# Kernel tuning notes

Measured on AMD Instinct MI355X. Metric: run time of the kernel, lower is better.

Reference implementation:

```python
import jax, jax.numpy as jnp
import numpy as np

HEADS = 30
HEAD_DIM = 64
DIM = HEADS * HEAD_DIM  # 1920
TXT = 226
VID = 2048
EPS = 1e-5


def setup_inputs() -> dict:
    key = jax.random.key(0)
    ks = jax.random.split(key, 12)
    s = 1.0 / np.sqrt(DIM)
    return {
        "hidden_states": jax.random.normal(ks[0], (1, VID, DIM), jnp.float32),
        "encoder_hidden_states": jax.random.normal(ks[1], (1, TXT, DIM), jnp.float32),
        "rope_cos": jax.random.uniform(ks[2], (VID, HEAD_DIM), jnp.float32, -1.0, 1.0),
        "rope_sin": jax.random.uniform(ks[3], (VID, HEAD_DIM), jnp.float32, -1.0, 1.0),
        "Wq": jax.random.normal(ks[4], (DIM, DIM), jnp.float32) * s,
        "bq": jnp.zeros((DIM,), jnp.float32),
        "Wk": jax.random.normal(ks[5], (DIM, DIM), jnp.float32) * s,
        "bk": jnp.zeros((DIM,), jnp.float32),
        "Wv": jax.random.normal(ks[6], (DIM, DIM), jnp.float32) * s,
        "bv": jnp.zeros((DIM,), jnp.float32),
        "ln_q_w": jnp.ones((HEAD_DIM,), jnp.float32),
        "ln_q_b": jnp.zeros((HEAD_DIM,), jnp.float32),
        "ln_k_w": jnp.ones((HEAD_DIM,), jnp.float32),
        "ln_k_b": jnp.zeros((HEAD_DIM,), jnp.float32),
        "Wo": jax.random.normal(ks[7], (DIM, DIM), jnp.float32) * s,
        "bo": jnp.zeros((DIM,), jnp.float32),
    }


def _layernorm(x, w, b):
    mu = jnp.mean(x, axis=-1, keepdims=True)
    var = jnp.var(x, axis=-1, keepdims=True)
    return (x - mu) * jax.lax.rsqrt(var + EPS) * w + b


def _apply_rope(x, cos, sin):
    # x: [B,H,S_vid,D]; cos/sin: [S_vid,D]. Interleaved-pair rotation (diffusers use_real, unbind_dim=-1).
    xr = x[..., 0::2]
    xi = x[..., 1::2]
    rot = jnp.stack([-xi, xr], axis=-1).reshape(x.shape)
    return x * cos + rot * sin


def reference(hidden_states, encoder_hidden_states, rope_cos, rope_sin,
              Wq, bq, Wk, bk, Wv, bv, ln_q_w, ln_q_b, ln_k_w, ln_k_b, Wo, bo):
    T = encoder_hidden_states.shape[1]
    h = jnp.concatenate([encoder_hidden_states, hidden_states], axis=1)  # [B,S,D]
    B, S, _ = h.shape

    def proj(W, bias):
        y = h @ W.T + bias
        return y.reshape(B, S, HEADS, HEAD_DIM).transpose(0, 2, 1, 3)  # [B,H,S,d]

    q = proj(Wq, bq)
    k = proj(Wk, bk)
    v = proj(Wv, bv)

    q = _layernorm(q, ln_q_w, ln_q_b)
    k = _layernorm(k, ln_k_w, ln_k_b)

    # rotary embedding applied only to the image/video tokens
    q = jnp.concatenate([q[:, :, :T], _apply_rope(q[:, :, T:], rope_cos, rope_sin)], axis=2)
    k = jnp.concatenate([k[:, :, :T], _apply_rope(k[:, :, T:], rope_cos, rope_sin)], axis=2)

    scale = 1.0 / np.sqrt(HEAD_DIM)
    scores = jnp.einsum("bhqd,bhkd->bhqk", q, k) * scale
    attn = jax.nn.softmax(scores, axis=-1)
    out = jnp.einsum("bhqk,bhkd->bhqd", attn, v)

    out = out.transpose(0, 2, 1, 3).reshape(B, S, DIM)
    out = out @ Wo.T + bo
    return out[:, T:], out[:, :T]
```

## Files before the change

### kernel.cpp

```cpp
#include <hip/hip_runtime.h>
#include <hip/hip_bf16.h>

typedef __hip_bfloat16 bf16;
using f32x4 = __attribute__((ext_vector_type(4))) float;
using f32x16 = __attribute__((ext_vector_type(16))) float;
using s16x8 = __attribute__((ext_vector_type(8))) short;

#define S_TOT 2274
#define S_PAD 2304
#define TTXT 226
#define DIMN 1920
#define NH 30
#define HD 64
#define NQKV 5760
#define QSCALE 0.1803368801f
#define NSPLIT 3
#define SMAX 20.0f

#define GLOAD_LDS16(g, l)                                                              \
  __builtin_amdgcn_global_load_lds((const __attribute__((address_space(1))) void*)(g), \
                                   (__attribute__((address_space(3))) void*)(l), 16, 0, 0)

__global__ void k_prep_all(const float* __restrict__ hid, const float* __restrict__ enc,
                           const float* __restrict__ Wq, const float* __restrict__ Wk,
                           const float* __restrict__ Wv, const float* __restrict__ Wo,
                           bf16* __restrict__ h_bf, bf16* __restrict__ wqkv,
                           bf16* __restrict__ wo_bf) {
  const long T1 = (long)S_PAD * DIMN;
  const long PER = (long)DIMN * DIMN;
  long i4 = ((long)blockIdx.x * blockDim.x + threadIdx.x) * 4;
  if (i4 >= T1 + 4 * PER) return;
  float4 v = make_float4(0.f, 0.f, 0.f, 0.f);
  bf16* dst;
  long di;
  if (i4 < T1) {
    int s = (int)(i4 / DIMN);
    if (s < TTXT)
      v = *reinterpret_cast<const float4*>(enc + i4);
    else if (s < S_TOT)
      v = *reinterpret_cast<const float4*>(hid + i4 - (long)TTXT * DIMN);
    dst = h_bf;
    di = i4;
  } else if (i4 < T1 + 3 * PER) {
    const long j = i4 - T1;
    const float* src = (j < PER) ? (Wq + j) : (j < 2 * PER) ? (Wk + j - PER) : (Wv + j - 2 * PER);
    v = *reinterpret_cast<const float4*>(src);
    dst = wqkv;
    di = j;
  } else {
    const long j = i4 - T1 - 3 * PER;
    v = *reinterpret_cast<const float4*>(Wo + j);
    dst = wo_bf;
    di = j;
  }
  union {
    bf16 b[4];
    short4 s4;
  } o;
  o.b[0] = __float2bfloat16(v.x);
  o.b[1] = __float2bfloat16(v.y);
  o.b[2] = __float2bfloat16(v.z);
  o.b[3] = __float2bfloat16(v.w);
  *reinterpret_cast<short4*>(dst + di) = o.s4;
}

#define NKT32 60
#define QBUF 24576
__global__ __launch_bounds__(512, 4) void k_gemm_qkv9(
    const bf16* __restrict__ A, const bf16* __restrict__ B, const float* __restrict__ bq,
    const float* __restrict__ bk, const float* __restrict__ bv, const float* __restrict__ lqw,
    const float* __restrict__ lqb, const float* __restrict__ lkw, const float* __restrict__ lkb,
    const float* __restrict__ cosT, const float* __restrict__ sinT, bf16* __restrict__ qb,
    bf16* __restrict__ kbf, bf16* __restrict__ vt) {
  __shared__ __align__(16) char smem[3 * QBUF];
  const int tid = threadIdx.x;
  const int w = tid >> 6, lane = tid & 63;
  const int clo = lane & 15, lhi = lane >> 4;
  const int wr = w >> 1, wc = w & 1;
  const int m0 = blockIdx.y * 256, n0 = blockIdx.x * 128;

  const int u1 = 512 + tid;
  const long ga0 = (long)(m0 + (tid >> 2)) * DIMN + (((tid & 3) ^ ((tid >> 2) & 3)) * 8);
  const long ga1 = (long)(m0 + (u1 >> 2)) * DIMN + (((u1 & 3) ^ ((u1 >> 2) & 3)) * 8);
  const long gb0 = (long)(n0 + (tid >> 2)) * DIMN + (((tid & 3) ^ ((tid >> 2) & 3)) * 8);
  const int wbase = w * 1024;

  auto stage = [&](int b, int kt) {
    char* Ab = &smem[b * QBUF];
    char* Bb = Ab + 16384;
    const int ko = kt * 32;
    GLOAD_LDS16(A + ga0 + ko, Ab + wbase);
    GLOAD_LDS16(A + ga1 + ko, Ab + 8192 + wbase);
    GLOAD_LDS16(B + gb0 + ko, Bb + wbase);
  };

  auto rdf = [&](const char* base, int row) {
    return *reinterpret_cast<const s16x8*>(base + row * 64 + ((lhi ^ (row & 3)) * 16));
  };

  f32x4 acc[4][4] = {};

  stage(0, 0);
  stage(1, 1);
  for (int t = 0; t < NKT32; ++t) {
    if (t < NKT32 - 1)
      asm volatile("s_waitcnt vmcnt(3)" ::: "memory");
    else
      asm volatile("s_waitcnt vmcnt(0)" ::: "memory");
    __builtin_amdgcn_s_barrier();
    if (t + 2 < NKT32) stage((t + 2) % 3, t + 2);
    const char* Ab = &smem[(t % 3) * QBUF];
    const char* Bb = Ab + 16384;
    s16x8 af[4], bfr[4];
#pragma unroll
    for (int m = 0; m < 4; ++m) af[m] = rdf(Ab, wr * 64 + m * 16 + clo);
#pragma unroll
    for (int n = 0; n < 4; ++n) bfr[n] = rdf(Bb, wc * 64 + n * 16 + clo);
    __builtin_amdgcn_s_setprio(1);
#pragma unroll
    for (int m = 0; m < 4; ++m)
#pragma unroll
      for (int n = 0; n < 4; ++n)
        acc[m][n] = __builtin_amdgcn_mfma_f32_16x16x32_bf16(af[m], bfr[n], acc[m][n], 0, 0, 0);
    __builtin_amdgcn_s_setprio(0);
  }
  __syncthreads();

  const int gcol0 = n0 + wc * 64;
  const int sect = gcol0 / DIMN;
  const int hcol = gcol0 - sect * DIMN;
  const int head = hcol >> 6;
  const int row0 = m0 + wr * 64;

  if (sect < 2) {
    const float* bias = sect ? bk : bq;
    const float* lw = sect ? lkw : lqw;
    const float* lb = sect ? lkb : lqb;
    bf16* dst = sect ? kbf : qb;
    const float oscale = sect ? 1.f : QSCALE;
    float bb[4], lww[4], lbb[4];
#pragma unroll
    for (int n = 0; n < 4; ++n) {
      const int d = (n << 4) + clo;
      bb[n] = bias[hcol + d];
      lww[n] = lw[d];
      lbb[n] = lb[d];
    }
#pragma unroll
    for (int m = 0; m < 4; ++m) {
#pragma unroll
      for (int r = 0; r < 4; ++r) {
        const int row = row0 + m * 16 + lhi * 4 + r;
        float x[4];
#pragma unroll
        for (int n = 0; n < 4; ++n) x[n] = acc[m][n][r] + bb[n];
        float s_ = (x[0] + x[1]) + (x[2] + x[3]);
        float q_ = x[0] * x[0];
        q_ = fmaf(x[1], x[1], q_);
        q_ = fmaf(x[2], x[2], q_);
        q_ = fmaf(x[3], x[3], q_);
#pragma unroll
        for (int off = 1; off <= 8; off <<= 1) {
          s_ += __shfl_xor(s_, off);
          q_ += __shfl_xor(q_, off);
        }
        const float mu = s_ * (1.f / 64.f);
        const float var = q_ * (1.f / 64.f) - mu * mu;
        const float rst = rsqrtf(var + 1e-5f);
        float xn[4];
#pragma unroll
        for (int n = 0; n < 4; ++n) xn[n] = (x[n] - mu) * rst * lww[n] + lbb[n];
        const bool dorope = (row >= TTXT) && (row < S_TOT);
        if (dorope) {
          const float* cr = cosT + (long)(row - TTXT) * HD;
          const float* sr2 = sinT + (long)(row - TTXT) * HD;
#pragma unroll
          for (int n = 0; n < 4; ++n) {
            const int d = (n << 4) + clo;
            const float p = __shfl_xor(xn[n], 1);
            xn[n] = xn[n] * cr[d] + ((clo & 1) ? p : -p) * sr2[d];
          }
        }
#pragma unroll
        for (int n = 0; n < 4; ++n)
          dst[((long)head * S_PAD + row) * HD + (n << 4) + clo] =
              __float2bfloat16(xn[n] * oscale);
      }
    }
  } else {
    float bb[4];
#pragma unroll
    for (int n = 0; n < 4; ++n) bb[n] = bv[hcol + (n << 4) + clo];
    bf16* Lp = reinterpret_cast<bf16*>(smem + w * 9216);
#pragma unroll
    for (int m = 0; m < 4; ++m)
#pragma unroll
      for (int n = 0; n < 4; ++n)
#pragma unroll
        for (int r = 0; r < 4; ++r)
          Lp[((n << 4) + clo) * 72 + m * 16 + lhi * 4 + r] =
              __float2bfloat16(acc[m][n][r] + bb[n]);
    const int dsub = lane >> 3, sc = lane & 7;
#pragma unroll
    for (int it = 0; it < 8; ++it) {
      const int d = it * 8 + dsub;
      s16x8 v = *reinterpret_cast<const s16x8*>(&Lp[d * 72 + sc * 8]);
      *reinterpret_cast<s16x8*>(vt + ((long)head * HD + d) * S_PAD + row0 + sc * 8) = v;
    }
  }
}

__global__ __launch_bounds__(256, 4) void k_gemm_proj9(const bf16* __restrict__ A,
                                                       const bf16* __restrict__ B,
                                                       float* __restrict__ C,
                                                       const float* __restrict__ bias) {
  __shared__ __align__(16) char smem[3 * 12288];
  const int tid = threadIdx.x;
  const int w = tid >> 6, lane = tid & 63;
  const int clo = lane & 15, lhi = lane >> 4;
  const int wr = w >> 1, wc = w & 1;
  const int m0 = blockIdx.y * 128, n0 = blockIdx.x * 64;

  const int u1 = 256 + tid;
  const long ga0 = (long)(m0 + (tid >> 2)) * DIMN + (((tid & 3) ^ ((tid >> 2) & 3)) * 8);
  const long ga1 = (long)(m0 + (u1 >> 2)) * DIMN + (((u1 & 3) ^ ((u1 >> 2) & 3)) * 8);
  const long gb0 = (long)(n0 + (tid >> 2)) * DIMN + (((tid & 3) ^ ((tid >> 2) & 3)) * 8);
  const int wbase = w * 1024;

  auto stage = [&](int b, int kt) {
    char* Ab = &smem[b * 12288];
    char* Bb = Ab + 8192;
    const int ko = kt * 32;
    GLOAD_LDS16(A + ga0 + ko, Ab + wbase);
    GLOAD_LDS16(A + ga1 + ko, Ab + 4096 + wbase);
    GLOAD_LDS16(B + gb0 + ko, Bb + wbase);
  };

  auto rdf = [&](const char* base, int row) {
    return *reinterpret_cast<const s16x8*>(base + row * 64 + ((lhi ^ (row & 3)) * 16));
  };

  f32x4 acc[4][2] = {};

  stage(0, 0);
  stage(1, 1);
  for (int t = 0; t < NKT32; ++t) {
    if (t < NKT32 - 1)
      asm volatile("s_waitcnt vmcnt(3)" ::: "memory");
    else
      asm volatile("s_waitcnt vmcnt(0)" ::: "memory");
    __builtin_amdgcn_s_barrier();
    if (t + 2 < NKT32) stage((t + 2) % 3, t + 2);
    const char* Ab = &smem[(t % 3) * 12288];
    const char* Bb = Ab + 8192;
    s16x8 af[4], bfr[2];
#pragma unroll
    for (int m = 0; m < 4; ++m) af[m] = rdf(Ab, wr * 64 + m * 16 + clo);
#pragma unroll
    for (int n = 0; n < 2; ++n) bfr[n] = rdf(Bb, wc * 32 + n * 16 + clo);
    __builtin_amdgcn_s_setprio(1);
#pragma unroll
    for (int m = 0; m < 4; ++m)
#pragma unroll
      for (int n = 0; n < 2; ++n)
        acc[m][n] = __builtin_amdgcn_mfma_f32_16x16x32_bf16(af[m], bfr[n], acc[m][n], 0, 0, 0);
    __builtin_amdgcn_s_setprio(0);
  }
#pragma unroll
  for (int n = 0; n < 2; ++n) {
    const int col = n0 + wc * 32 + n * 16 + clo;
    const float bvv = bias[col];
#pragma unroll
    for (int m = 0; m < 4; ++m) {
#pragma unroll
      for (int r = 0; r < 4; ++r) {
        const int row = m0 + wr * 64 + m * 16 + lhi * 4 + r;
        if (row < S_TOT) {
          const int dst = (row >= TTXT) ? (row - TTXT) : (row + (S_TOT - TTXT));
          C[(long)dst * DIMN + col] = acc[m][n][r] + bvv;
        }
      }
    }
  }
}

__global__ __launch_bounds__(512, 4) void k_flash11(const bf16* __restrict__ qb,
                                                    const bf16* __restrict__ kbf,
                                                    const bf16* __restrict__ vt,
                                                    float* __restrict__ po,
                                                    float* __restrict__ pl) {
  __shared__ __align__(16) char smem[32768];
  const int h = blockIdx.x, qt = blockIdx.y, ks = blockIdx.z;
  const int tid = threadIdx.x, w = tid >> 6, lane = tid & 63;
  const int l31 = lane & 31, hf = lane >> 5;
  const bf16* Qh = qb + (long)h * S_PAD * HD;
  const bf16* Kh = kbf + (long)h * S_PAD * HD;
  const bf16* Vh = vt + (long)h * HD * S_PAD;
  const int q0w = qt * 256 + w * 32;
  const int T0 = ks * 12;

  s16x8 qf[4];
#pragma unroll
  for (int t = 0; t < 4; ++t)
    qf[t] = *reinterpret_cast<const s16x8*>(Qh + (long)(q0w + l31) * HD + t * 16 + hf * 8);

  f32x16 accO[2] = {};
  f32x16 lacc = {};

  const s16x8 ones8 = {0x3F80, 0x3F80, 0x3F80, 0x3F80, 0x3F80, 0x3F80, 0x3F80, 0x3F80};

  const int sr = tid >> 3, sc8 = tid & 7;
  const long kg0 = (long)sr * HD + ((sc8 ^ (sr & 7)) * 8);
  const long vg0 = (long)sr * S_PAD + ((sc8 ^ (sr & 7)) * 8);
  const int ldsb = w * 1024;

  auto stage = [&](int b, int kb0) {
    char* Kb = &smem[b * 16384];
    char* Vb = &smem[b * 16384 + 8192];
    GLOAD_LDS16(Kh + (long)kb0 * HD + kg0, Kb + ldsb);
    GLOAD_LDS16(Vh + kb0 + vg0, Vb + ldsb);
  };

  auto ldsrd = [&](const char* base, int row, int c) {
    return *reinterpret_cast<const s16x8*>(base + row * 128 + ((c ^ (row & 7)) * 16));
  };
  auto pk2 = [&](float a, float b) -> unsigned {
    __hip_bfloat162 t = __float22bfloat162_rn(make_float2(a, b));
    return *reinterpret_cast<unsigned*>(&t);
  };

  stage(0, T0 * 64);
  __syncthreads();
  int cur = 0;
  for (int kt = 0; kt < 12; ++kt) {
    const int kb0 = (T0 + kt) * 64;
    if (kt + 1 < 12) stage(cur ^ 1, kb0 + 64);
    const char* Kb = &smem[cur * 16384];
    const char* Vb = &smem[cur * 16384 + 8192];

    f32x16 s0 = {}, s1 = {};
#pragma unroll
    for (int t = 0; t < 4; ++t) {
      s16x8 k0 = ldsrd(Kb, l31, 2 * t + hf);
      s16x8 k1 = ldsrd(Kb, 32 + l31, 2 * t + hf);
      s0 = __builtin_amdgcn_mfma_f32_32x32x16_bf16(k0, qf[t], s0, 0, 0, 0);
      s1 = __builtin_amdgcn_mfma_f32_32x32x16_bf16(k1, qf[t], s1, 0, 0, 0);
    }
    if (kb0 + 64 > S_TOT) {
#pragma unroll
      for (int j = 0; j < 16; ++j) {
        const int key = kb0 + (j & 3) + 8 * (j >> 2) + 4 * hf;
        if (key >= S_TOT) s0[j] = -1e30f;
        if (key + 32 >= S_TOT) s1[j] = -1e30f;
      }
    }
#pragma unroll
    for (int j = 0; j < 16; ++j) {
      s0[j] = exp2f(s0[j] - SMAX);
      s1[j] = exp2f(s1[j] - SMAX);
    }
    unsigned gw0[8], gw1[8];
#pragma unroll
    for (int i = 0; i < 4; ++i) {
      gw0[2 * i] = pk2(s0[4 * i], s0[4 * i + 1]);
      gw0[2 * i + 1] = pk2(s0[4 * i + 2], s0[4 * i + 3]);
      gw1[2 * i] = pk2(s1[4 * i], s1[4 * i + 1]);
      gw1[2 * i + 1] = pk2(s1[4 * i + 2], s1[4 * i + 3]);
    }
    s16x8 pa[4];
#pragma unroll
    for (int b = 0; b < 2; ++b) {
      unsigned* gw = b ? gw1 : gw0;
#pragma unroll
      for (int t = 0; t < 2; ++t) {
        auto rA = __builtin_amdgcn_permlane32_swap(gw[4 * t + 0], gw[4 * t + 2], false, false);
        auto rB = __builtin_amdgcn_permlane32_swap(gw[4 * t + 1], gw[4 * t + 3], false, false);
        union {
          unsigned u[4];
          s16x8 v;
        } A;
        A.u[0] = rA[0];
        A.u[1] = rB[0];
        A.u[2] = rA[1];
        A.u[3] = rB[1];
        pa[b * 2 + t] = A.v;
      }
    }
#pragma unroll
    for (int t4 = 0; t4 < 4; ++t4) {
      s16x8 v0 = ldsrd(Vb, l31, 2 * t4 + hf);
      s16x8 v1 = ldsrd(Vb, 32 + l31, 2 * t4 + hf);
      accO[0] = __builtin_amdgcn_mfma_f32_32x32x16_bf16(pa[t4], v0, accO[0], 0, 0, 0);
      accO[1] = __builtin_amdgcn_mfma_f32_32x32x16_bf16(pa[t4], v1, accO[1], 0, 0, 0);
      lacc = __builtin_amdgcn_mfma_f32_32x32x16_bf16(pa[t4], ones8, lacc, 0, 0, 0);
    }
    __syncthreads();
    cur ^= 1;
  }
  const long rowbase = ((long)(ks * NH + h)) * S_PAD + q0w;
  if (l31 == 0) {
#pragma unroll
    for (int j = 0; j < 16; ++j) pl[rowbase + (j & 3) + 8 * (j >> 2) + 4 * hf] = lacc[j];
  }
#pragma unroll
  for (int j = 0; j < 16; ++j) {
    const int pat = (j & 3) + 8 * (j >> 2) + 4 * hf;
    float* dst = po + (rowbase + pat) * HD + l31;
    dst[0] = accO[0][j];
    dst[32] = accO[1][j];
  }
}

__global__ __launch_bounds__(256) void k_combine3(const float* __restrict__ po,
                                                  const float* __restrict__ pl,
                                                  bf16* __restrict__ ao) {
  const int idx = blockIdx.x * 256 + threadIdx.x;
  const int d4 = (idx & 15) * 4;
  const int row = (idx >> 4) % S_PAD;
  const int h = idx / (S_PAD * 16);
  if (row >= S_TOT) return;
  float4 o = make_float4(0.f, 0.f, 0.f, 0.f);
  float l = 0.f;
#pragma unroll
  for (int i = 0; i < NSPLIT; ++i) {
    const long r = ((long)(i * NH + h)) * S_PAD + row;
    const float4 p = *reinterpret_cast<const float4*>(po + r * HD + d4);
    o.x += p.x;
    o.y += p.y;
    o.z += p.z;
    o.w += p.w;
    l += pl[r];
  }
  const float inv = 1.f / l;
  union {
    bf16 b[4];
    short4 s4;
  } ob;
  ob.b[0] = __float2bfloat16(o.x * inv);
  ob.b[1] = __float2bfloat16(o.y * inv);
  ob.b[2] = __float2bfloat16(o.z * inv);
  ob.b[3] = __float2bfloat16(o.w * inv);
  *reinterpret_cast<short4*>(ao + (long)row * DIMN + h * HD + d4) = ob.s4;
}

extern "C" void kernel_launch(void* const* d_in, const int* in_sizes, int n_in, void* d_out,
                              int out_size, void* d_ws, size_t ws_size, hipStream_t stream) {
  const float* hid = (const float*)d_in[0];
  const float* enc = (const float*)d_in[1];
  const float* rc = (const float*)d_in[2];
  const float* rs = (const float*)d_in[3];
  const float* Wq = (const float*)d_in[4];
  const float* bq = (const float*)d_in[5];
  const float* Wk = (const float*)d_in[6];
  const float* bk = (const float*)d_in[7];
  const float* Wv = (const float*)d_in[8];
  const float* bv = (const float*)d_in[9];
  const float* lqw = (const float*)d_in[10];
  const float* lqb = (const float*)d_in[11];
  const float* lkw = (const float*)d_in[12];
  const float* lkb = (const float*)d_in[13];
  const float* Wo = (const float*)d_in[14];
  const float* bo = (const float*)d_in[15];
  float* out = (float*)d_out;

  char* ws = (char*)d_ws;
  size_t off = 0;
  float* po = (float*)(ws + off);
  off += (size_t)NSPLIT * NH * S_PAD * HD * 4;
  bf16* h_bf = (bf16*)(ws + off);
  off += (size_t)S_PAD * DIMN * 2;
  bf16* wqkv = (bf16*)(ws + off);
  off += (size_t)3 * DIMN * DIMN * 2;
  bf16* wo = (bf16*)(ws + off);
  off += (size_t)DIMN * DIMN * 2;
  bf16* q_bf = (bf16*)(ws + off);
  off += (size_t)NH * S_PAD * HD * 2;
  bf16* k_bf = (bf16*)(ws + off);
  off += (size_t)NH * S_PAD * HD * 2;
  bf16* vt_bf = (bf16*)(ws + off);
  off += (size_t)NH * HD * S_PAD * 2;
  bf16* at_bf = (bf16*)(ws + off);
  off += (size_t)S_PAD * DIMN * 2;

  float* pl = (float*)h_bf;

  const long PREP_N = ((long)S_PAD * DIMN + 4L * DIMN * DIMN) / 4;
  k_prep_all<<<(int)((PREP_N + 255) / 256), 256, 0, stream>>>(hid, enc, Wq, Wk, Wv, Wo, h_bf,
                                                              wqkv, wo);
  k_gemm_qkv9<<<dim3(NQKV / 128, S_PAD / 256), 512, 0, stream>>>(
      h_bf, wqkv, bq, bk, bv, lqw, lqb, lkw, lkb, rc, rs, q_bf, k_bf, vt_bf);
  k_flash11<<<dim3(NH, S_PAD / 256, NSPLIT), 512, 0, stream>>>(q_bf, k_bf, vt_bf, po, pl);
  k_combine3<<<NH * S_PAD * 16 / 256, 256, 0, stream>>>(po, pl, at_bf);
  k_gemm_proj9<<<dim3(DIMN / 64, S_PAD / 128), 256, 0, stream>>>(at_bf, wo, out, bo);
}
```

Before: 221.0 us.

## Add XCD-aware block swizzle, change LDS swizzle, 4-way KV split with bf16 partials

Remaps GEMM workgroup IDs so that neighbouring tiles land on the same XCD, which should improve L2 reuse of shared A and B tiles. Changes the LDS XOR swizzle to key on row>>1 to cut bank conflicts on the 64-byte rows. Raises the flash-attention KV split from 3 to 4 (9 KV tiles each) to get more parallelism, and stores the partial outputs as bf16 instead of fp32 to halve partial-result traffic into the combine kernel. The bf16 partials lose some precision before the split results are summed.

```diff
diff --git a/kernel.cpp b/kernel.cpp
--- a/kernel.cpp
+++ b/kernel.cpp
@@ -14,12 +14,18 @@
 #define HD 64
 #define NQKV 5760
 #define QSCALE 0.1803368801f
-#define NSPLIT 3
+#define NSPLIT 4
 #define SMAX 20.0f
 
 #define GLOAD_LDS16(g, l)                                                              \
   __builtin_amdgcn_global_load_lds((const __attribute__((address_space(1))) void*)(g), \
                                    (__attribute__((address_space(3))) void*)(l), 16, 0, 0)
+
+__device__ __forceinline__ int xcd_swz(int orig, int nwg) {
+  const int q = nwg >> 3, r = nwg & 7;
+  const int xcd = orig & 7, pos = orig >> 3;
+  return (xcd < r ? xcd * (q + 1) : r * (q + 1) + (xcd - r) * q) + pos;
+}
 
 __global__ void k_prep_all(const float* __restrict__ hid, const float* __restrict__ enc,
                            const float* __restrict__ Wq, const float* __restrict__ Wk,
@@ -66,7 +72,7 @@
 
 #define NKT32 60
 #define QBUF 24576
-__global__ __launch_bounds__(512, 4) void k_gemm_qkv9(
+__global__ __launch_bounds__(512, 4) void k_gemm_qkv11(
     const bf16* __restrict__ A, const bf16* __restrict__ B, const float* __restrict__ bq,
     const float* __restrict__ bk, const float* __restrict__ bv, const float* __restrict__ lqw,
     const float* __restrict__ lqb, const float* __restrict__ lkw, const float* __restrict__ lkb,
@@ -77,12 +83,13 @@
   const int w = tid >> 6, lane = tid & 63;
   const int clo = lane & 15, lhi = lane >> 4;
   const int wr = w >> 1, wc = w & 1;
-  const int m0 = blockIdx.y * 256, n0 = blockIdx.x * 128;
+  const int swz = xcd_swz(blockIdx.y * 45 + blockIdx.x, 405);
+  const int m0 = (swz / 45) * 256, n0 = (swz % 45) * 128;
 
   const int u1 = 512 + tid;
-  const long ga0 = (long)(m0 + (tid >> 2)) * DIMN + (((tid & 3) ^ ((tid >> 2) & 3)) * 8);
-  const long ga1 = (long)(m0 + (u1 >> 2)) * DIMN + (((u1 & 3) ^ ((u1 >> 2) & 3)) * 8);
-  const long gb0 = (long)(n0 + (tid >> 2)) * DIMN + (((tid & 3) ^ ((tid >> 2) & 3)) * 8);
+  const long ga0 = (long)(m0 + (tid >> 2)) * DIMN + (((tid & 3) ^ ((tid >> 3) & 3)) * 8);
+  const long ga1 = (long)(m0 + (u1 >> 2)) * DIMN + (((u1 & 3) ^ ((u1 >> 3) & 3)) * 8);
+  const long gb0 = (long)(n0 + (tid >> 2)) * DIMN + (((tid & 3) ^ ((tid >> 3) & 3)) * 8);
   const int wbase = w * 1024;
 
   auto stage = [&](int b, int kt) {
@@ -95,7 +102,7 @@
   };
 
   auto rdf = [&](const char* base, int row) {
-    return *reinterpret_cast<const s16x8*>(base + row * 64 + ((lhi ^ (row & 3)) * 16));
+    return *reinterpret_cast<const s16x8*>(base + row * 64 + ((lhi ^ ((row >> 1) & 3)) * 16));
   };
 
   f32x4 acc[4][4] = {};
@@ -210,21 +217,22 @@
   }
 }
 
-__global__ __launch_bounds__(256, 4) void k_gemm_proj9(const bf16* __restrict__ A,
-                                                       const bf16* __restrict__ B,
-                                                       float* __restrict__ C,
-                                                       const float* __restrict__ bias) {
+__global__ __launch_bounds__(256, 4) void k_gemm_proj11(const bf16* __restrict__ A,
+                                                        const bf16* __restrict__ B,
+                                                        float* __restrict__ C,
+                                                        const float* __restrict__ bias) {
   __shared__ __align__(16) char smem[3 * 12288];
   const int tid = threadIdx.x;
   const int w = tid >> 6, lane = tid & 63;
   const int clo = lane & 15, lhi = lane >> 4;
   const int wr = w >> 1, wc = w & 1;
-  const int m0 = blockIdx.y * 128, n0 = blockIdx.x * 64;
+  const int swz = xcd_swz(blockIdx.y * 30 + blockIdx.x, 540);
+  const int m0 = (swz / 30) * 128, n0 = (swz % 30) * 64;
 
   const int u1 = 256 + tid;
-  const long ga0 = (long)(m0 + (tid >> 2)) * DIMN + (((tid & 3) ^ ((tid >> 2) & 3)) * 8);
-  const long ga1 = (long)(m0 + (u1 >> 2)) * DIMN + (((u1 & 3) ^ ((u1 >> 2) & 3)) * 8);
-  const long gb0 = (long)(n0 + (tid >> 2)) * DIMN + (((tid & 3) ^ ((tid >> 2) & 3)) * 8);
+  const long ga0 = (long)(m0 + (tid >> 2)) * DIMN + (((tid & 3) ^ ((tid >> 3) & 3)) * 8);
+  const long ga1 = (long)(m0 + (u1 >> 2)) * DIMN + (((u1 & 3) ^ ((u1 >> 3) & 3)) * 8);
+  const long gb0 = (long)(n0 + (tid >> 2)) * DIMN + (((tid & 3) ^ ((tid >> 3) & 3)) * 8);
   const int wbase = w * 1024;
 
   auto stage = [&](int b, int kt) {
@@ -237,7 +245,7 @@
   };
 
   auto rdf = [&](const char* base, int row) {
-    return *reinterpret_cast<const s16x8*>(base + row * 64 + ((lhi ^ (row & 3)) * 16));
+    return *reinterpret_cast<const s16x8*>(base + row * 64 + ((lhi ^ ((row >> 1) & 3)) * 16));
   };
 
   f32x4 acc[4][2] = {};
@@ -284,10 +292,10 @@
   }
 }
 
-__global__ __launch_bounds__(512, 4) void k_flash11(const bf16* __restrict__ qb,
+__global__ __launch_bounds__(512, 4) void k_flash14(const bf16* __restrict__ qb,
                                                     const bf16* __restrict__ kbf,
                                                     const bf16* __restrict__ vt,
-                                                    float* __restrict__ po,
+                                                    bf16* __restrict__ po,
                                                     float* __restrict__ pl) {
   __shared__ __align__(16) char smem[32768];
   const int h = blockIdx.x, qt = blockIdx.y, ks = blockIdx.z;
@@ -297,7 +305,7 @@
   const bf16* Kh = kbf + (long)h * S_PAD * HD;
   const bf16* Vh = vt + (long)h * HD * S_PAD;
   const int q0w = qt * 256 + w * 32;
-  const int T0 = ks * 12;
+  const int T0 = ks * 9;
 
   s16x8 qf[4];
 #pragma unroll
@@ -332,9 +340,9 @@
   stage(0, T0 * 64);
   __syncthreads();
   int cur = 0;
-  for (int kt = 0; kt < 12; ++kt) {
+  for (int kt = 0; kt < 9; ++kt) {
     const int kb0 = (T0 + kt) * 64;
-    if (kt + 1 < 12) stage(cur ^ 1, kb0 + 64);
+    if (kt + 1 < 9) stage(cur ^ 1, kb0 + 64);
     const char* Kb = &smem[cur * 16384];
     const char* Vb = &smem[cur * 16384 + 8192];
 
@@ -405,13 +413,13 @@
 #pragma unroll
   for (int j = 0; j < 16; ++j) {
     const int pat = (j & 3) + 8 * (j >> 2) + 4 * hf;
-    float* dst = po + (rowbase + pat) * HD + l31;
-    dst[0] = accO[0][j];
-    dst[32] = accO[1][j];
-  }
-}
-
-__global__ __launch_bounds__(256) void k_combine3(const float* __restrict__ po,
+    bf16* dst = po + (rowbase + pat) * HD + l31;
+    dst[0] = __float2bfloat16(accO[0][j]);
+    dst[32] = __float2bfloat16(accO[1][j]);
+  }
+}
+
+__global__ __launch_bounds__(256) void k_combine4(const bf16* __restrict__ po,
                                                   const float* __restrict__ pl,
                                                   bf16* __restrict__ ao) {
   const int idx = blockIdx.x * 256 + threadIdx.x;
@@ -419,16 +427,16 @@
   const int row = (idx >> 4) % S_PAD;
   const int h = idx / (S_PAD * 16);
   if (row >= S_TOT) return;
-  float4 o = make_float4(0.f, 0.f, 0.f, 0.f);
+  float o[4] = {0.f, 0.f, 0.f, 0.f};
   float l = 0.f;
 #pragma unroll
   for (int i = 0; i < NSPLIT; ++i) {
     const long r = ((long)(i * NH + h)) * S_PAD + row;
-    const float4 p = *reinterpret_cast<const float4*>(po + r * HD + d4);
-    o.x += p.x;
-    o.y += p.y;
-    o.z += p.z;
-    o.w += p.w;
+    const ushort4 p = *reinterpret_cast<const ushort4*>(po + r * HD + d4);
+    o[0] += __uint_as_float((unsigned)p.x << 16);
+    o[1] += __uint_as_float((unsigned)p.y << 16);
+    o[2] += __uint_as_float((unsigned)p.z << 16);
+    o[3] += __uint_as_float((unsigned)p.w << 16);
     l += pl[r];
   }
   const float inv = 1.f / l;
@@ -436,10 +444,8 @@
     bf16 b[4];
     short4 s4;
   } ob;
-  ob.b[0] = __float2bfloat16(o.x * inv);
-  ob.b[1] = __float2bfloat16(o.y * inv);
-  ob.b[2] = __float2bfloat16(o.z * inv);
-  ob.b[3] = __float2bfloat16(o.w * inv);
+#pragma unroll
+  for (int i = 0; i < 4; ++i) ob.b[i] = __float2bfloat16(o[i] * inv);
   *reinterpret_cast<short4*>(ao + (long)row * DIMN + h * HD + d4) = ob.s4;
 }
 
@@ -465,8 +471,8 @@
 
   char* ws = (char*)d_ws;
   size_t off = 0;
-  float* po = (float*)(ws + off);
-  off += (size_t)NSPLIT * NH * S_PAD * HD * 4;
+  bf16* po = (bf16*)(ws + off);
+  off += (size_t)S_PAD * NQKV * 4;
   bf16* h_bf = (bf16*)(ws + off);
   off += (size_t)S_PAD * DIMN * 2;
   bf16* wqkv = (bf16*)(ws + off);
@@ -487,9 +493,9 @@
   const long PREP_N = ((long)S_PAD * DIMN + 4L * DIMN * DIMN) / 4;
   k_prep_all<<<(int)((PREP_N + 255) / 256), 256, 0, stream>>>(hid, enc, Wq, Wk, Wv, Wo, h_bf,
                                                               wqkv, wo);
-  k_gemm_qkv9<<<dim3(NQKV / 128, S_PAD / 256), 512, 0, stream>>>(
-      h_bf, wqkv, bq, bk, bv, lqw, lqb, lkw, lkb, rc, rs, q_bf, k_bf, vt_bf);
-  k_flash11<<<dim3(NH, S_PAD / 256, NSPLIT), 512, 0, stream>>>(q_bf, k_bf, vt_bf, po, pl);
-  k_combine3<<<NH * S_PAD * 16 / 256, 256, 0, stream>>>(po, pl, at_bf);
-  k_gemm_proj9<<<dim3(DIMN / 64, S_PAD / 128), 256, 0, stream>>>(at_bf, wo, out, bo);
-}
+  k_gemm_qkv11<<<dim3(45, 9), 512, 0, stream>>>(h_bf, wqkv, bq, bk, bv, lqw, lqb, lkw, lkb, rc,
+                                                rs, q_bf, k_bf, vt_bf);
+  k_flash14<<<dim3(NH, S_PAD / 256, NSPLIT), 512, 0, stream>>>(q_bf, k_bf, vt_bf, po, pl);
+  k_combine4<<<NH * S_PAD * 16 / 256, 256, 0, stream>>>(po, pl, at_bf);
+  k_gemm_proj11<<<dim3(30, 18), 256, 0, stream>>>(at_bf, wo, out, bo);
+}
```

Result: faster. 213.3 us (median of 2 runs) (-3.5%).
